# Kernel optimization log

Hardware: AMD Instinct MI355X
Metric: run time of the kernel (lower is better)

Reference implementation:

```python
import jax, jax.numpy as jnp
import numpy as np

B, H, W, C = 4, 64, 64, 64


def conv1x1(x, w, b):
    # 1x1 conv on channels_last input == per-pixel dense layer
    return jnp.einsum('bhwc,cd->bhwd', x, w) + b


def setup_inputs() -> dict:
    key = jax.random.key(0)
    ks = jax.random.split(key, 8)
    std = 1.0 / np.sqrt(C)
    inp = {
        'x': jax.random.normal(ks[0], (B, H, W, C), dtype=jnp.float32),
        'wq_s': jax.random.normal(ks[1], (C, C), dtype=jnp.float32) * std,
        'bq_s': jnp.zeros((C,), jnp.float32),
        'wk_s': jax.random.normal(ks[2], (C, C), dtype=jnp.float32) * std,
        'bk_s': jnp.zeros((C,), jnp.float32),
        'wv_s': jax.random.normal(ks[3], (C, C), dtype=jnp.float32) * std,
        'bv_s': jnp.zeros((C,), jnp.float32),
        'wq_c': jax.random.normal(ks[4], (C, C), dtype=jnp.float32) * std,
        'bq_c': jnp.zeros((C,), jnp.float32),
        'wk_c': jax.random.normal(ks[5], (C, C), dtype=jnp.float32) * std,
        'bk_c': jnp.zeros((C,), jnp.float32),
        'wv_c': jax.random.normal(ks[6], (C, C), dtype=jnp.float32) * std,
        'bv_c': jnp.zeros((C,), jnp.float32),
        'a': jnp.float32(0.0),
        'b': jnp.float32(0.0),
    }
    return inp


def reference(x, wq_s, bq_s, wk_s, bk_s, wv_s, bv_s,
              wq_c, bq_c, wk_c, bk_c, wv_c, bv_c, a, b):
    scale = jnp.sqrt(jnp.float32(C))
    N = H * W

    # ---- Spatial self-attention: tokens = pixels, (B, HW, C) ----
    qs = conv1x1(x, wq_s, bq_s).reshape(B, N, C)
    ks_ = conv1x1(x, wk_s, bk_s).reshape(B, N, C)
    vs = conv1x1(x, wv_s, bv_s).reshape(B, N, C)
    att_s = jax.nn.softmax(jnp.einsum('bnc,bmc->bnm', qs, ks_) / scale, axis=-1)
    spat = jnp.einsum('bnm,bmc->bnc', att_s, vs).reshape(B, H, W, C)

    # ---- Channel self-attention ----
    # Faithful to the TF code: raw reshape of channels_last (B,H,W,C) -> (B,C,HW)
    # (a memory reinterpretation, NOT a transpose).
    qc = conv1x1(x, wq_c, bq_c).reshape(B, C, N)
    kc = conv1x1(x, wk_c, bk_c).reshape(B, C, N)
    vc = conv1x1(x, wv_c, bv_c).reshape(B, C, N)
    att_c = jax.nn.softmax(jnp.einsum('bcn,bdn->bcd', qc, kc) / scale, axis=-1)
    chan = jnp.einsum('bcd,bdn->bcn', att_c, vc).reshape(B, H, W, C)

    # ---- Scaled residual fusion ----
    return (b * spat + x) + (a * chan + x)
```

## Files before the change

kernel.cpp:

```cpp
#include <hip/hip_runtime.h>

#define NTOK 4096
#define PSTR 72

typedef short bf16x8 __attribute__((ext_vector_type(8)));
typedef short bf16x4 __attribute__((ext_vector_type(4)));
typedef float f32x4 __attribute__((ext_vector_type(4)));

__device__ __forceinline__ short f2bf(float f) {
  union { float f; unsigned u; } v; v.f = f;
  unsigned r = v.u + 0x7fffu + ((v.u >> 16) & 1u);
  return (short)(r >> 16);
}
__device__ __forceinline__ short f2bf_t(float f) {
  union { float f; unsigned u; } v; v.f = f;
  return (short)(v.u >> 16);
}
__device__ __forceinline__ float bf2f(short s) {
  union { unsigned u; float f; } v; v.u = ((unsigned)(unsigned short)s) << 16;
  return v.f;
}

struct ConvArgs {
  const float* x;
  const float* w[6];
  const float* bias[6];
  short* out[6];
};

__global__ __launch_bounds__(256) void conv_qkv(ConvArgs args) {
  __shared__ __align__(16) short lWt[6][64*PSTR];
  __shared__ float lB[6*64];
  __shared__ __align__(16) short lT[64*PSTR];
  const int tid = threadIdx.x;
  const int wave = tid >> 6, lane = tid & 63;
  const int quad = lane >> 4, l16 = lane & 15;
  const float QSC = 0.125f * 1.44269504088896f;

  for (int wi = 0; wi < 6; wi++) {
    const f32x4* wsrc = (const f32x4*)args.w[wi];
    for (int u0 = 0; u0 < 4; u0++) {
      int u = u0 * 256 + tid;
      int c = u >> 4, d4 = u & 15;
      f32x4 v = wsrc[u];
      for (int j = 0; j < 4; j++)
        lWt[wi][(d4*4+j)*PSTR + c] = f2bf(v[j]);
    }
  }
  if (tid < 64)
    for (int wi = 0; wi < 6; wi++) lB[wi*64 + tid] = args.bias[wi][tid];

  int row = blockIdx.x * 64 + wave*16 + l16;
  const float* xr = args.x + (size_t)row*64 + quad*8;
  f32x4 x0 = *(const f32x4*)xr;
  f32x4 x1 = *(const f32x4*)(xr+4);
  f32x4 x2 = *(const f32x4*)(xr+32);
  f32x4 x3 = *(const f32x4*)(xr+36);
  bf16x8 a0, a1;
  for (int j=0;j<4;j++){ a0[j]=f2bf(x0[j]); a0[4+j]=f2bf(x1[j]); a1[j]=f2bf(x2[j]); a1[4+j]=f2bf(x3[j]); }
  __syncthreads();

  int orow_base = blockIdx.x*64 + wave*16 + quad*4;
  for (int wi=0; wi<6; wi++) {
    for (int dt=0; dt<4; dt++) {
      bf16x8 b0 = *(const bf16x8*)&lWt[wi][(dt*16+l16)*PSTR + quad*8];
      bf16x8 b1 = *(const bf16x8*)&lWt[wi][(dt*16+l16)*PSTR + 32 + quad*8];
      f32x4 acc = {0.f,0.f,0.f,0.f};
      acc = __builtin_amdgcn_mfma_f32_16x16x32_bf16(a0, b0, acc, 0,0,0);
      acc = __builtin_amdgcn_mfma_f32_16x16x32_bf16(a1, b1, acc, 0,0,0);
      float bias = lB[wi*64 + dt*16 + l16];
      if (wi == 0) {
        short* outp = args.out[0];
        for (int r=0;r<4;r++)
          outp[(size_t)(orow_base + r)*64 + dt*16 + l16] = f2bf((acc[r] + bias)*QSC);
      } else if (wi != 2) {
        short* outp = args.out[wi];
        for (int r=0;r<4;r++)
          outp[(size_t)(orow_base + r)*64 + dt*16 + l16] = f2bf(acc[r] + bias);
      } else {
        for (int r=0;r<4;r++)
          lT[(dt*16+l16)*PSTR + wave*16 + quad*4 + r] = f2bf(acc[r] + bias);
      }
    }
  }
  __syncthreads();
  int b  = (blockIdx.x*64) >> 12;
  int n0 = (blockIdx.x*64) & 4095;
  for (int u0=0; u0<2; u0++) {
    int u = u0*256 + tid;
    int c = u >> 3, t8 = u & 7;
    *(bf16x8*)(args.out[2] + (size_t)(b*64+c)*4096 + n0 + t8*8) =
        *(const bf16x8*)&lT[c*PSTR + t8*8];
  }
}

__global__ __launch_bounds__(256, 2) void attn_part(const short* __restrict__ qs,
    const short* __restrict__ ks, const short* __restrict__ vst,
    short* __restrict__ opart, float* __restrict__ ml) {
  __shared__ __align__(16) short sK[2][64*PSTR];
  __shared__ __align__(16) short sV[2][64*PSTR];
  __shared__ __align__(16) short sP[4][16*PSTR];
  const int tid = threadIdx.x;
  const int wave = tid>>6, lane = tid&63, quad = lane>>4, l16 = lane&15;
  const int qtile = blockIdx.x*4 + wave;
  const int batch = blockIdx.y, kg = blockIdx.z;
  const int srow = tid >> 3, sc8 = tid & 7;

  const short* kb  = ks  + (size_t)batch*NTOK*64;
  const short* vtb = vst + (size_t)batch*64*NTOK;
  const int k0base = kg*512;

  bf16x8 qa[4][2];
  {
    const short* qp = qs + ((size_t)batch*NTOK + qtile*64)*64;
    for (int qg=0;qg<4;qg++) {
      qa[qg][0] = *(const bf16x8*)(qp + (qg*16+l16)*64 + quad*8);
      qa[qg][1] = *(const bf16x8*)(qp + (qg*16+l16)*64 + 32 + quad*8);
    }
  }

  f32x4 ot[4][4];
  for (int qg=0;qg<4;qg++) for (int ct=0;ct<4;ct++) ot[qg][ct]=(f32x4){0.f,0.f,0.f,0.f};
  float mq[4] = {-1e30f,-1e30f,-1e30f,-1e30f};
  float lq[4] = {0.f,0.f,0.f,0.f};

  {
    int k0 = k0base;
    for (int h=0;h<2;h++) {
      int row = (h*256+tid)>>3, c8 = (h*256+tid)&7;
      bf16x8 gk = *(const bf16x8*)(kb + (size_t)(k0+row)*64 + c8*8);
      bf16x8 gv = *(const bf16x8*)(vtb + (size_t)row*4096 + k0 + c8*8);
      *(bf16x8*)&sK[0][row*PSTR + c8*8] = gk;
      *(bf16x8*)&sV[0][row*PSTR + c8*8] = gv;
    }
  }
  __syncthreads();

  for (int t=0; t<8; t++) {
    const int cur = t & 1;
    bf16x8 gk0, gk1, gv0, gv1;
    if (t < 7) {
      int k0 = k0base + (t+1)*64;
      int row0 = srow, row1 = 32 + srow;
      gk0 = *(const bf16x8*)(kb + (size_t)(k0+row0)*64 + sc8*8);
      gv0 = *(const bf16x8*)(vtb + (size_t)row0*4096 + k0 + sc8*8);
      gk1 = *(const bf16x8*)(kb + (size_t)(k0+row1)*64 + sc8*8);
      gv1 = *(const bf16x8*)(vtb + (size_t)row1*4096 + k0 + sc8*8);
    }

    bf16x8 kf[4][2], vf[4][2];
    for (int mt=0;mt<4;mt++) {
      kf[mt][0] = *(const bf16x8*)&sK[cur][(mt*16+l16)*PSTR + quad*8];
      kf[mt][1] = *(const bf16x8*)&sK[cur][(mt*16+l16)*PSTR + 32 + quad*8];
      vf[mt][0] = *(const bf16x8*)&sV[cur][(mt*16+l16)*PSTR + quad*8];
      vf[mt][1] = *(const bf16x8*)&sV[cur][(mt*16+l16)*PSTR + 32 + quad*8];
    }

    for (int qg=0;qg<4;qg++) {
      f32x4 st[4];
      for (int mt=0;mt<4;mt++) {
        f32x4 z = {0.f,0.f,0.f,0.f};
        z = __builtin_amdgcn_mfma_f32_16x16x32_bf16(kf[mt][0], qa[qg][0], z, 0,0,0);
        z = __builtin_amdgcn_mfma_f32_16x16x32_bf16(kf[mt][1], qa[qg][1], z, 0,0,0);
        st[mt] = z;
      }
      float mx = st[0][0];
      for (int mt=0;mt<4;mt++)
        for (int r=0;r<4;r++) mx = fmaxf(mx, st[mt][r]);
      mx = fmaxf(mx, __shfl_xor(mx, 16));
      mx = fmaxf(mx, __shfl_xor(mx, 32));
      float mnew = fmaxf(mq[qg], mx);
      float al = __builtin_amdgcn_exp2f(mq[qg] - mnew);
      float sum = 0.f;
      for (int mt=0;mt<4;mt++)
        for (int r=0;r<4;r++) {
          float p = __builtin_amdgcn_exp2f(st[mt][r] - mnew);
          st[mt][r] = p; sum += p;
        }
      lq[qg] = lq[qg]*al + sum;
      mq[qg] = mnew;
      for (int ct=0;ct<4;ct++)
        for (int r=0;r<4;r++) ot[qg][ct][r] *= al;
      short* lPw = sP[wave];
      for (int mt=0;mt<4;mt++) {
        bf16x4 pk;
        for (int r=0;r<4;r++) pk[r] = f2bf_t(st[mt][r]);
        *(bf16x4*)&lPw[l16*PSTR + mt*16 + quad*4] = pk;
      }
      bf16x8 pb0 = *(const bf16x8*)&lPw[l16*PSTR + quad*8];
      bf16x8 pb1 = *(const bf16x8*)&lPw[l16*PSTR + 32 + quad*8];
      for (int ct=0;ct<4;ct++) {
        ot[qg][ct] = __builtin_amdgcn_mfma_f32_16x16x32_bf16(vf[ct][0], pb0, ot[qg][ct], 0,0,0);
        ot[qg][ct] = __builtin_amdgcn_mfma_f32_16x16x32_bf16(vf[ct][1], pb1, ot[qg][ct], 0,0,0);
      }
    }

    if (t < 7) {
      int nxt = cur ^ 1;
      int row0 = srow, row1 = 32 + srow;
      *(bf16x8*)&sK[nxt][row0*PSTR + sc8*8] = gk0;
      *(bf16x8*)&sV[nxt][row0*PSTR + sc8*8] = gv0;
      *(bf16x8*)&sK[nxt][row1*PSTR + sc8*8] = gk1;
      *(bf16x8*)&sV[nxt][row1*PSTR + sc8*8] = gv1;
    }
    __syncthreads();
  }

  size_t obase = (((size_t)batch*64 + qtile)*8 + kg) * 4096;
  for (int qg=0;qg<4;qg++)
    for (int ct=0;ct<4;ct++) {
      bf16x4 pk;
      for (int r=0;r<4;r++) pk[r] = f2bf(ot[qg][ct][r]);
      *(bf16x4*)&opart[obase + (size_t)(qg*1024 + ct*256 + quad*64 + l16*4)] = pk;
    }
  float lt[4];
  for (int qg=0;qg<4;qg++) {
    float s = lq[qg];
    s += __shfl_xor(s, 16);
    s += __shfl_xor(s, 32);
    lt[qg] = s;
  }
  if (quad == 0) {
    float* mlp = ml + (((size_t)batch*64 + qtile)*8 + kg)*128;
    for (int qg=0;qg<4;qg++) {
      mlp[qg*16 + l16]      = mq[qg];
      mlp[64 + qg*16 + l16] = lt[qg];
    }
  }
}

__global__ __launch_bounds__(256) void chan_qk_part(const short* __restrict__ qc,
    const short* __restrict__ kc, float* __restrict__ Gpart) {
  const int tid = threadIdx.x;
  const int wave = tid>>6, lane = tid&63, quad = lane>>4, l16 = lane&15;
  const int ks_ = blockIdx.x, b = blockIdx.y;
  const int n0 = ks_*64;
  const short* qb = qc + (size_t)b*NTOK*64;
  const short* kb = kc + (size_t)b*NTOK*64;

  bf16x8 aq0 = *(const bf16x8*)(qb + (size_t)(wave*16+l16)*4096 + n0 + quad*8);
  bf16x8 aq1 = *(const bf16x8*)(qb + (size_t)(wave*16+l16)*4096 + n0 + 32 + quad*8);
  f32x4 acc[4];
  for (int nt=0;nt<4;nt++) {
    bf16x8 bk0 = *(const bf16x8*)(kb + (size_t)(nt*16+l16)*4096 + n0 + quad*8);
    bf16x8 bk1 = *(const bf16x8*)(kb + (size_t)(nt*16+l16)*4096 + n0 + 32 + quad*8);
    f32x4 z = {0.f,0.f,0.f,0.f};
    z = __builtin_amdgcn_mfma_f32_16x16x32_bf16(aq0, bk0, z, 0,0,0);
    z = __builtin_amdgcn_mfma_f32_16x16x32_bf16(aq1, bk1, z, 0,0,0);
    acc[nt] = z;
  }
  float* gp = Gpart + ((size_t)b*64 + ks_)*4096;
  for (int nt=0;nt<4;nt++)
    for (int r=0;r<4;r++)
      gp[(wave*16 + quad*4 + r)*64 + nt*16 + l16] = acc[nt][r];
}

__global__ __launch_bounds__(256) void chan_reduce_sm(const float* __restrict__ Gpart,
    float* __restrict__ att) {
  const int cg = blockIdx.x, b = blockIdx.y, t = threadIdx.x;
  const int c = cg*16 + (t>>4), dq = t & 15;
  const float* gp = Gpart + (size_t)b*64*4096 + c*64 + dq*4;
  f32x4 acc = {0.f,0.f,0.f,0.f};
  for (int ks_=0; ks_<64; ks_++)
    acc += *(const f32x4*)(gp + (size_t)ks_*4096);
  const float SC = 0.125f * 1.44269504088896f;
  f32x4 v;
  for (int j=0;j<4;j++) v[j] = acc[j]*SC;
  float mx = fmaxf(fmaxf(v[0],v[1]), fmaxf(v[2],v[3]));
  mx = fmaxf(mx, __shfl_xor(mx, 1));
  mx = fmaxf(mx, __shfl_xor(mx, 2));
  mx = fmaxf(mx, __shfl_xor(mx, 4));
  mx = fmaxf(mx, __shfl_xor(mx, 8));
  f32x4 p; float sum = 0.f;
  for (int j=0;j<4;j++){ p[j] = __builtin_amdgcn_exp2f(v[j]-mx); sum += p[j]; }
  sum += __shfl_xor(sum, 1);
  sum += __shfl_xor(sum, 2);
  sum += __shfl_xor(sum, 4);
  sum += __shfl_xor(sum, 8);
  float inv = 1.f/sum;
  f32x4 r; for (int j=0;j<4;j++) r[j] = p[j]*inv;
  *(f32x4*)(att + (size_t)b*4096 + c*64 + dq*4) = r;
}

__global__ __launch_bounds__(256) void chan_av(const float* __restrict__ att,
    const short* __restrict__ vc, float* __restrict__ chan) {
  __shared__ float lA[4096];
  const int tid = threadIdx.x;
  const int batch = blockIdx.y, ch = blockIdx.x;
  for (int i=tid;i<4096;i+=256) lA[i] = att[batch*4096+i];
  __syncthreads();
  const int n = ch*64 + (tid & 63);
  const int cg = tid >> 6;
  const short* vb = vc + (size_t)batch*NTOK*64;
  float acc[16];
  for (int i=0;i<16;i++) acc[i]=0.f;
  for (int d=0;d<64;d++) {
    float v = bf2f(vb[(size_t)d*4096 + n]);
    for (int ci=0;ci<16;ci++) acc[ci] += lA[(cg*16+ci)*64 + d] * v;
  }
  float* cb = chan + (size_t)batch*NTOK*64;
  for (int ci=0;ci<16;ci++) cb[(size_t)(cg*16+ci)*4096 + n] = acc[ci];
}

__global__ __launch_bounds__(256) void combine_fuse(const short* __restrict__ opart,
    const float* __restrict__ ml, const float* __restrict__ chan,
    const float* __restrict__ x, const float* __restrict__ pa,
    const float* __restrict__ pb, float* __restrict__ out) {
  __shared__ float sW[8][64];
  const int qt = blockIdx.x, b = blockIdx.y, t = threadIdx.x;
  const size_t base = ((size_t)b*64 + qt)*8;
  if (t < 64) {
    const int q = t;
    float m[8], l[8];
    for (int kg=0;kg<8;kg++) {
      m[kg] = ml[(base+kg)*128 + q];
      l[kg] = ml[(base+kg)*128 + 64 + q];
    }
    float M = m[0];
    for (int kg=1;kg<8;kg++) M = fmaxf(M, m[kg]);
    float den = 0.f, w[8];
    for (int kg=0;kg<8;kg++){ w[kg] = __builtin_amdgcn_exp2f(m[kg]-M); den += w[kg]*l[kg]; }
    float inv = 1.f/den;
    for (int kg=0;kg<8;kg++) sW[kg][q] = w[kg]*inv;
  }
  __syncthreads();
  const int ct = t>>6, quad = (t>>4)&3, l16 = t&15;
  const float av = pa[0], bv = pb[0];
  for (int qg=0;qg<4;qg++) {
    const int q = qg*16 + l16;
    f32x4 acc = {0.f,0.f,0.f,0.f};
    for (int kg=0;kg<8;kg++) {
      bf16x4 chunk = *(const bf16x4*)&opart[(base+kg)*4096 + qg*1024 + ct*256 + quad*64 + l16*4];
      float w = sW[kg][q];
      for (int r=0;r<4;r++) acc[r] += w*bf2f(chunk[r]);
    }
    size_t flat = ((size_t)b*NTOK + qt*64 + q)*64 + ct*16 + quad*4;
    f32x4 xv = *(const f32x4*)(x + flat);
    f32x4 cv = *(const f32x4*)(chan + flat);
    f32x4 r;
    for (int j=0;j<4;j++) r[j] = bv*acc[j] + av*cv[j] + 2.f*xv[j];
    *(f32x4*)(out + flat) = r;
  }
}

extern "C" void kernel_launch(void* const* d_in, const int* in_sizes, int n_in,
                              void* d_out, int out_size, void* d_ws, size_t ws_size,
                              hipStream_t stream) {
  const float* x = (const float*)d_in[0];
  char* ws = (char*)d_ws;
  const size_t MB = 1048576;
  short* qs    = (short*)(ws + 0*MB);
  short* ks_   = (short*)(ws + 2*MB);
  short* vst   = (short*)(ws + 4*MB);
  short* qc    = (short*)(ws + 6*MB);
  short* kc    = (short*)(ws + 8*MB);
  short* vc    = (short*)(ws + 10*MB);
  short* opart = (short*)(ws + 12*MB);
  float* ml    = (float*)(ws + 28*MB);
  float* att   = (float*)(ws + 29*MB);
  float* Gpart = (float*)(ws + 0*MB);
  float* chan  = (float*)(ws + 4*MB);

  ConvArgs ca;
  ca.x = x;
  for (int i=0;i<6;i++) {
    ca.w[i]    = (const float*)d_in[1+2*i];
    ca.bias[i] = (const float*)d_in[2+2*i];
  }
  ca.out[0]=qs; ca.out[1]=ks_; ca.out[2]=vst;
  ca.out[3]=qc; ca.out[4]=kc; ca.out[5]=vc;

  hipLaunchKernelGGL(conv_qkv, dim3(256), dim3(256), 0, stream, ca);
  hipLaunchKernelGGL(attn_part, dim3(16,4,8), dim3(256), 0, stream, qs, ks_, vst, opart, ml);
  hipLaunchKernelGGL(chan_qk_part, dim3(64,4), dim3(256), 0, stream, qc, kc, Gpart);
  hipLaunchKernelGGL(chan_reduce_sm, dim3(4,4), dim3(256), 0, stream, Gpart, att);
  hipLaunchKernelGGL(chan_av, dim3(64,4), dim3(256), 0, stream, att, vc, chan);
  hipLaunchKernelGGL(combine_fuse, dim3(64,4), dim3(256), 0, stream,
                     opart, ml, chan, x, (const float*)d_in[13], (const float*)d_in[14],
                     (float*)d_out);
}
```

Baseline: 151.5 us.

## Pre-transpose weights once, split attention waves across more blocks, fuse channel AV into combine

A new prep_w kernel converts the six weight matrices to transposed bf16 once, with the Q scale folded in. conv_qkv then reads them straight from global memory instead of every block rebuilding them in LDS. attn_part now gives each wave two query groups instead of four, doubling the grid and raising the occupancy hint to 3 for more parallelism and fewer registers, but each block reloads the same K/V tiles for half as many queries. The chan_av kernel is removed and its matrix-vector product is folded into combine_fuse, so the fp32 chan intermediate is never written or read back, at the cost of more per-thread work in the combine step.

```diff
diff --git a/kernel.cpp b/kernel.cpp
--- a/kernel.cpp
+++ b/kernel.cpp
@@ -21,34 +21,40 @@
   return v.f;
 }
 
+struct PrepArgs {
+  const float* w[6];
+  short* wt;
+};
+
 struct ConvArgs {
   const float* x;
-  const float* w[6];
+  const short* wt;
   const float* bias[6];
   short* out[6];
 };
 
+#define QSC (0.125f * 1.44269504088896f)
+
+__global__ __launch_bounds__(256) void prep_w(PrepArgs p) {
+  const int wi = blockIdx.x;
+  const float* w = p.w[wi];
+  short* o = p.wt + wi*4096;
+  const int d = threadIdx.x & 63, cb = (threadIdx.x >> 6) * 16;
+  const float sc = (wi == 0) ? QSC : 1.f;
+  bf16x8 v0, v1;
+  for (int j=0;j<8;j++) {
+    v0[j] = f2bf(w[(cb+j)*64 + d] * sc);
+    v1[j] = f2bf(w[(cb+8+j)*64 + d] * sc);
+  }
+  *(bf16x8*)(o + d*64 + cb)     = v0;
+  *(bf16x8*)(o + d*64 + cb + 8) = v1;
+}
+
 __global__ __launch_bounds__(256) void conv_qkv(ConvArgs args) {
-  __shared__ __align__(16) short lWt[6][64*PSTR];
-  __shared__ float lB[6*64];
   __shared__ __align__(16) short lT[64*PSTR];
   const int tid = threadIdx.x;
   const int wave = tid >> 6, lane = tid & 63;
   const int quad = lane >> 4, l16 = lane & 15;
-  const float QSC = 0.125f * 1.44269504088896f;
-
-  for (int wi = 0; wi < 6; wi++) {
-    const f32x4* wsrc = (const f32x4*)args.w[wi];
-    for (int u0 = 0; u0 < 4; u0++) {
-      int u = u0 * 256 + tid;
-      int c = u >> 4, d4 = u & 15;
-      f32x4 v = wsrc[u];
-      for (int j = 0; j < 4; j++)
-        lWt[wi][(d4*4+j)*PSTR + c] = f2bf(v[j]);
-    }
-  }
-  if (tid < 64)
-    for (int wi = 0; wi < 6; wi++) lB[wi*64 + tid] = args.bias[wi][tid];
 
   int row = blockIdx.x * 64 + wave*16 + l16;
   const float* xr = args.x + (size_t)row*64 + quad*8;
@@ -58,22 +64,19 @@
   f32x4 x3 = *(const f32x4*)(xr+36);
   bf16x8 a0, a1;
   for (int j=0;j<4;j++){ a0[j]=f2bf(x0[j]); a0[4+j]=f2bf(x1[j]); a1[j]=f2bf(x2[j]); a1[4+j]=f2bf(x3[j]); }
-  __syncthreads();
 
   int orow_base = blockIdx.x*64 + wave*16 + quad*4;
   for (int wi=0; wi<6; wi++) {
+    const short* wtp = args.wt + wi*4096;
     for (int dt=0; dt<4; dt++) {
-      bf16x8 b0 = *(const bf16x8*)&lWt[wi][(dt*16+l16)*PSTR + quad*8];
-      bf16x8 b1 = *(const bf16x8*)&lWt[wi][(dt*16+l16)*PSTR + 32 + quad*8];
+      bf16x8 b0 = *(const bf16x8*)(wtp + (dt*16+l16)*64 + quad*8);
+      bf16x8 b1 = *(const bf16x8*)(wtp + (dt*16+l16)*64 + 32 + quad*8);
       f32x4 acc = {0.f,0.f,0.f,0.f};
       acc = __builtin_amdgcn_mfma_f32_16x16x32_bf16(a0, b0, acc, 0,0,0);
       acc = __builtin_amdgcn_mfma_f32_16x16x32_bf16(a1, b1, acc, 0,0,0);
-      float bias = lB[wi*64 + dt*16 + l16];
-      if (wi == 0) {
-        short* outp = args.out[0];
-        for (int r=0;r<4;r++)
-          outp[(size_t)(orow_base + r)*64 + dt*16 + l16] = f2bf((acc[r] + bias)*QSC);
-      } else if (wi != 2) {
+      float bias = args.bias[wi][dt*16+l16];
+      if (wi == 0) bias *= QSC;
+      if (wi != 2) {
         short* outp = args.out[wi];
         for (int r=0;r<4;r++)
           outp[(size_t)(orow_base + r)*64 + dt*16 + l16] = f2bf(acc[r] + bias);
@@ -94,7 +97,7 @@
   }
 }
 
-__global__ __launch_bounds__(256, 2) void attn_part(const short* __restrict__ qs,
+__global__ __launch_bounds__(256, 3) void attn_part(const short* __restrict__ qs,
     const short* __restrict__ ks, const short* __restrict__ vst,
     short* __restrict__ opart, float* __restrict__ ml) {
   __shared__ __align__(16) short sK[2][64*PSTR];
@@ -102,7 +105,8 @@
   __shared__ __align__(16) short sP[4][16*PSTR];
   const int tid = threadIdx.x;
   const int wave = tid>>6, lane = tid&63, quad = lane>>4, l16 = lane&15;
-  const int qtile = blockIdx.x*4 + wave;
+  const int qtile = blockIdx.x*2 + (wave>>1);
+  const int qgo = (wave&1)*2;
   const int batch = blockIdx.y, kg = blockIdx.z;
   const int srow = tid >> 3, sc8 = tid & 7;
 
@@ -110,29 +114,22 @@
   const short* vtb = vst + (size_t)batch*64*NTOK;
   const int k0base = kg*512;
 
-  bf16x8 qa[4][2];
-  {
-    const short* qp = qs + ((size_t)batch*NTOK + qtile*64)*64;
-    for (int qg=0;qg<4;qg++) {
-      qa[qg][0] = *(const bf16x8*)(qp + (qg*16+l16)*64 + quad*8);
-      qa[qg][1] = *(const bf16x8*)(qp + (qg*16+l16)*64 + 32 + quad*8);
-    }
-  }
-
-  f32x4 ot[4][4];
-  for (int qg=0;qg<4;qg++) for (int ct=0;ct<4;ct++) ot[qg][ct]=(f32x4){0.f,0.f,0.f,0.f};
-  float mq[4] = {-1e30f,-1e30f,-1e30f,-1e30f};
-  float lq[4] = {0.f,0.f,0.f,0.f};
-
-  {
-    int k0 = k0base;
-    for (int h=0;h<2;h++) {
-      int row = (h*256+tid)>>3, c8 = (h*256+tid)&7;
-      bf16x8 gk = *(const bf16x8*)(kb + (size_t)(k0+row)*64 + c8*8);
-      bf16x8 gv = *(const bf16x8*)(vtb + (size_t)row*4096 + k0 + c8*8);
-      *(bf16x8*)&sK[0][row*PSTR + c8*8] = gk;
-      *(bf16x8*)&sV[0][row*PSTR + c8*8] = gv;
-    }
+  bf16x8 qa[2][2];
+  for (int qg=0;qg<2;qg++) {
+    const short* qp = qs + ((size_t)batch*NTOK + qtile*64 + (qgo+qg)*16 + l16)*64;
+    qa[qg][0] = *(const bf16x8*)(qp + quad*8);
+    qa[qg][1] = *(const bf16x8*)(qp + 32 + quad*8);
+  }
+
+  f32x4 ot[2][4];
+  for (int qg=0;qg<2;qg++) for (int ct=0;ct<4;ct++) ot[qg][ct]=(f32x4){0.f,0.f,0.f,0.f};
+  float mq[2] = {-1e30f,-1e30f};
+  float lq[2] = {0.f,0.f};
+
+  for (int h=0;h<2;h++) {
+    int row = (h*256+tid)>>3, c8 = (h*256+tid)&7;
+    *(bf16x8*)&sK[0][row*PSTR + c8*8] = *(const bf16x8*)(kb + (size_t)(k0base+row)*64 + c8*8);
+    *(bf16x8*)&sV[0][row*PSTR + c8*8] = *(const bf16x8*)(vtb + (size_t)row*4096 + k0base + c8*8);
   }
   __syncthreads();
 
@@ -141,11 +138,10 @@
     bf16x8 gk0, gk1, gv0, gv1;
     if (t < 7) {
       int k0 = k0base + (t+1)*64;
-      int row0 = srow, row1 = 32 + srow;
-      gk0 = *(const bf16x8*)(kb + (size_t)(k0+row0)*64 + sc8*8);
-      gv0 = *(const bf16x8*)(vtb + (size_t)row0*4096 + k0 + sc8*8);
-      gk1 = *(const bf16x8*)(kb + (size_t)(k0+row1)*64 + sc8*8);
-      gv1 = *(const bf16x8*)(vtb + (size_t)row1*4096 + k0 + sc8*8);
+      gk0 = *(const bf16x8*)(kb + (size_t)(k0+srow)*64 + sc8*8);
+      gv0 = *(const bf16x8*)(vtb + (size_t)srow*4096 + k0 + sc8*8);
+      gk1 = *(const bf16x8*)(kb + (size_t)(k0+32+srow)*64 + sc8*8);
+      gv1 = *(const bf16x8*)(vtb + (size_t)(32+srow)*4096 + k0 + sc8*8);
     }
 
     bf16x8 kf[4][2], vf[4][2];
@@ -156,7 +152,7 @@
       vf[mt][1] = *(const bf16x8*)&sV[cur][(mt*16+l16)*PSTR + 32 + quad*8];
     }
 
-    for (int qg=0;qg<4;qg++) {
+    for (int qg=0;qg<2;qg++) {
       f32x4 st[4];
       for (int mt=0;mt<4;mt++) {
         f32x4 z = {0.f,0.f,0.f,0.f};
@@ -197,24 +193,23 @@
 
     if (t < 7) {
       int nxt = cur ^ 1;
-      int row0 = srow, row1 = 32 + srow;
-      *(bf16x8*)&sK[nxt][row0*PSTR + sc8*8] = gk0;
-      *(bf16x8*)&sV[nxt][row0*PSTR + sc8*8] = gv0;
-      *(bf16x8*)&sK[nxt][row1*PSTR + sc8*8] = gk1;
-      *(bf16x8*)&sV[nxt][row1*PSTR + sc8*8] = gv1;
+      *(bf16x8*)&sK[nxt][srow*PSTR + sc8*8]      = gk0;
+      *(bf16x8*)&sV[nxt][srow*PSTR + sc8*8]      = gv0;
+      *(bf16x8*)&sK[nxt][(32+srow)*PSTR + sc8*8] = gk1;
+      *(bf16x8*)&sV[nxt][(32+srow)*PSTR + sc8*8] = gv1;
     }
     __syncthreads();
   }
 
   size_t obase = (((size_t)batch*64 + qtile)*8 + kg) * 4096;
-  for (int qg=0;qg<4;qg++)
+  for (int qg=0;qg<2;qg++)
     for (int ct=0;ct<4;ct++) {
       bf16x4 pk;
       for (int r=0;r<4;r++) pk[r] = f2bf(ot[qg][ct][r]);
-      *(bf16x4*)&opart[obase + (size_t)(qg*1024 + ct*256 + quad*64 + l16*4)] = pk;
-    }
-  float lt[4];
-  for (int qg=0;qg<4;qg++) {
+      *(bf16x4*)&opart[obase + (size_t)((qgo+qg)*1024 + ct*256 + quad*64 + l16*4)] = pk;
+    }
+  float lt[2];
+  for (int qg=0;qg<2;qg++) {
     float s = lq[qg];
     s += __shfl_xor(s, 16);
     s += __shfl_xor(s, 32);
@@ -222,9 +217,9 @@
   }
   if (quad == 0) {
     float* mlp = ml + (((size_t)batch*64 + qtile)*8 + kg)*128;
-    for (int qg=0;qg<4;qg++) {
-      mlp[qg*16 + l16]      = mq[qg];
-      mlp[64 + qg*16 + l16] = lt[qg];
+    for (int qg=0;qg<2;qg++) {
+      mlp[(qgo+qg)*16 + l16]      = mq[qg];
+      mlp[64 + (qgo+qg)*16 + l16] = lt[qg];
     }
   }
 }
@@ -282,32 +277,14 @@
   *(f32x4*)(att + (size_t)b*4096 + c*64 + dq*4) = r;
 }
 
-__global__ __launch_bounds__(256) void chan_av(const float* __restrict__ att,
-    const short* __restrict__ vc, float* __restrict__ chan) {
-  __shared__ float lA[4096];
-  const int tid = threadIdx.x;
-  const int batch = blockIdx.y, ch = blockIdx.x;
-  for (int i=tid;i<4096;i+=256) lA[i] = att[batch*4096+i];
-  __syncthreads();
-  const int n = ch*64 + (tid & 63);
-  const int cg = tid >> 6;
-  const short* vb = vc + (size_t)batch*NTOK*64;
-  float acc[16];
-  for (int i=0;i<16;i++) acc[i]=0.f;
-  for (int d=0;d<64;d++) {
-    float v = bf2f(vb[(size_t)d*4096 + n]);
-    for (int ci=0;ci<16;ci++) acc[ci] += lA[(cg*16+ci)*64 + d] * v;
-  }
-  float* cb = chan + (size_t)batch*NTOK*64;
-  for (int ci=0;ci<16;ci++) cb[(size_t)(cg*16+ci)*4096 + n] = acc[ci];
-}
-
 __global__ __launch_bounds__(256) void combine_fuse(const short* __restrict__ opart,
-    const float* __restrict__ ml, const float* __restrict__ chan,
-    const float* __restrict__ x, const float* __restrict__ pa,
-    const float* __restrict__ pb, float* __restrict__ out) {
+    const float* __restrict__ ml, const float* __restrict__ att,
+    const short* __restrict__ vc, const float* __restrict__ x,
+    const float* __restrict__ pa, const float* __restrict__ pb,
+    float* __restrict__ out) {
   __shared__ float sW[8][64];
-  const int qt = blockIdx.x, b = blockIdx.y, t = threadIdx.x;
+  __shared__ float sAtt[64];
+  const int qt = blockIdx.x, b = blockIdx.y, hz = blockIdx.z, t = threadIdx.x;
   const size_t base = ((size_t)b*64 + qt)*8;
   if (t < 64) {
     const int q = t;
@@ -322,25 +299,43 @@
     for (int kg=0;kg<8;kg++){ w[kg] = __builtin_amdgcn_exp2f(m[kg]-M); den += w[kg]*l[kg]; }
     float inv = 1.f/den;
     for (int kg=0;kg<8;kg++) sW[kg][q] = w[kg]*inv;
+    sAtt[t] = att[(size_t)b*4096 + qt*64 + t];
   }
   __syncthreads();
-  const int ct = t>>6, quad = (t>>4)&3, l16 = t&15;
+
+  const int e0 = hz*2048 + t*8;
+  const int q = e0 >> 6;
+  const int qg = q >> 4, l16 = q & 15;
+  const int seg = (t&7) >> 1, quad0 = (t&1)*2;
+
+  float accS[8];
+  for (int j=0;j<8;j++) accS[j]=0.f;
+  for (int kg=0;kg<8;kg++) {
+    float w = sW[kg][q];
+    const short* op = opart + (base+kg)*4096 + qg*1024 + seg*256 + l16*4;
+    bf16x4 c0 = *(const bf16x4*)(op + quad0*64);
+    bf16x4 c1 = *(const bf16x4*)(op + (quad0+1)*64);
+    for (int r=0;r<4;r++) { accS[r] += w*bf2f(c0[r]); accS[4+r] += w*bf2f(c1[r]); }
+  }
+  float accC[8];
+  for (int j=0;j<8;j++) accC[j]=0.f;
+  const short* vb = vc + (size_t)b*NTOK*64;
+  for (int d=0; d<64; d++) {
+    bf16x8 v = *(const bf16x8*)(vb + (size_t)d*4096 + e0);
+    float a = sAtt[d];
+    for (int j=0;j<8;j++) accC[j] += a*bf2f(v[j]);
+  }
   const float av = pa[0], bv = pb[0];
-  for (int qg=0;qg<4;qg++) {
-    const int q = qg*16 + l16;
-    f32x4 acc = {0.f,0.f,0.f,0.f};
-    for (int kg=0;kg<8;kg++) {
-      bf16x4 chunk = *(const bf16x4*)&opart[(base+kg)*4096 + qg*1024 + ct*256 + quad*64 + l16*4];
-      float w = sW[kg][q];
-      for (int r=0;r<4;r++) acc[r] += w*bf2f(chunk[r]);
-    }
-    size_t flat = ((size_t)b*NTOK + qt*64 + q)*64 + ct*16 + quad*4;
-    f32x4 xv = *(const f32x4*)(x + flat);
-    f32x4 cv = *(const f32x4*)(chan + flat);
-    f32x4 r;
-    for (int j=0;j<4;j++) r[j] = bv*acc[j] + av*cv[j] + 2.f*xv[j];
-    *(f32x4*)(out + flat) = r;
-  }
+  size_t flat = ((size_t)b*64 + qt)*4096 + e0;
+  f32x4 x0 = *(const f32x4*)(x + flat);
+  f32x4 x1 = *(const f32x4*)(x + flat + 4);
+  f32x4 r0, r1;
+  for (int j=0;j<4;j++) {
+    r0[j] = bv*accS[j]   + av*accC[j]   + 2.f*x0[j];
+    r1[j] = bv*accS[4+j] + av*accC[4+j] + 2.f*x1[j];
+  }
+  *(f32x4*)(out + flat)     = r0;
+  *(f32x4*)(out + flat + 4) = r1;
 }
 
 extern "C" void kernel_launch(void* const* d_in, const int* in_sizes, int n_in,
@@ -358,24 +353,26 @@
   short* opart = (short*)(ws + 12*MB);
   float* ml    = (float*)(ws + 28*MB);
   float* att   = (float*)(ws + 29*MB);
+  short* wt    = (short*)(ws + 30*MB);
   float* Gpart = (float*)(ws + 0*MB);
-  float* chan  = (float*)(ws + 4*MB);
-
+
+  PrepArgs pa;
   ConvArgs ca;
-  ca.x = x;
+  ca.x = x; ca.wt = wt;
   for (int i=0;i<6;i++) {
-    ca.w[i]    = (const float*)d_in[1+2*i];
+    pa.w[i]    = (const float*)d_in[1+2*i];
     ca.bias[i] = (const float*)d_in[2+2*i];
   }
+  pa.wt = wt;
   ca.out[0]=qs; ca.out[1]=ks_; ca.out[2]=vst;
   ca.out[3]=qc; ca.out[4]=kc; ca.out[5]=vc;
 
+  hipLaunchKernelGGL(prep_w, dim3(6), dim3(256), 0, stream, pa);
   hipLaunchKernelGGL(conv_qkv, dim3(256), dim3(256), 0, stream, ca);
-  hipLaunchKernelGGL(attn_part, dim3(16,4,8), dim3(256), 0, stream, qs, ks_, vst, opart, ml);
+  hipLaunchKernelGGL(attn_part, dim3(32,4,8), dim3(256), 0, stream, qs, ks_, vst, opart, ml);
   hipLaunchKernelGGL(chan_qk_part, dim3(64,4), dim3(256), 0, stream, qc, kc, Gpart);
   hipLaunchKernelGGL(chan_reduce_sm, dim3(4,4), dim3(256), 0, stream, Gpart, att);
-  hipLaunchKernelGGL(chan_av, dim3(64,4), dim3(256), 0, stream, att, vc, chan);
-  hipLaunchKernelGGL(combine_fuse, dim3(64,4), dim3(256), 0, stream,
-                     opart, ml, chan, x, (const float*)d_in[13], (const float*)d_in[14],
+  hipLaunchKernelGGL(combine_fuse, dim3(64,4,2), dim3(256), 0, stream,
+                     opart, ml, att, vc, x, (const float*)d_in[13], (const float*)d_in[14],
                      (float*)d_out);
 }
```

Result: faster. 145.7 us (-3.8%).
